# Kernel optimization log

Hardware: AMD Instinct MI355X
Metric: run time of the kernel (lower is better)

Reference implementation:

```python
import jax, jax.numpy as jnp
import numpy as np

N_NODES = 50000
N_EDGES = 262144
EMBED = 512
FF = 1024
N_GRAPHS = 64
EPS = 1e-12  # F.normalize default eps


def setup_inputs() -> dict:
    key = jax.random.key(0)
    ks = jax.random.split(key, 12)
    d_in = 3 * EMBED
    s1 = 1.0 / np.sqrt(d_in)
    s2 = 1.0 / np.sqrt(FF)
    return {
        "x": jax.random.normal(ks[0], (N_NODES + N_EDGES, EMBED), jnp.float32),
        "pos": jax.random.normal(ks[1], (N_NODES, 3), jnp.float32),
        "W1e": jax.random.uniform(ks[2], (d_in, FF), jnp.float32, -s1, s1),
        "b1e": jax.random.uniform(ks[3], (FF,), jnp.float32, -s1, s1),
        "W2e": jax.random.uniform(ks[4], (FF, 1), jnp.float32, -s2, s2),
        "b2e": jax.random.uniform(ks[5], (1,), jnp.float32, -s2, s2),
        "W1f": jax.random.uniform(ks[6], (d_in, FF), jnp.float32, -s1, s1),
        "b1f": jax.random.uniform(ks[7], (FF,), jnp.float32, -s1, s1),
        "W2f": jax.random.uniform(ks[8], (FF, 1), jnp.float32, -s2, s2),
        "b2f": jax.random.uniform(ks[9], (1,), jnp.float32, -s2, s2),
        "batch": jnp.sort(jax.random.randint(ks[10], (N_NODES,), 0, N_GRAPHS, jnp.int32)),
        "edge_index": jax.random.randint(ks[11], (2, N_EDGES), 0, N_NODES, jnp.int32),
    }


def _mlp(h, W1, b1, W2, b2):
    return jax.nn.gelu(h @ W1 + b1) @ W2 + b2


def reference(x, pos, W1e, b1e, W2e, b2e, W1f, b1f, W2f, b2f, batch, edge_index):
    n_nodes = pos.shape[0]
    n_edges = edge_index.shape[1]
    src, dst = edge_index[0], edge_index[1]
    # edge-token rows of x live right after the node rows
    edge_tok = jax.lax.dynamic_slice_in_dim(x, n_nodes, n_edges, axis=0)
    inputs = jnp.concatenate([x[src], x[dst], edge_tok], axis=-1)  # [E, 3*D]
    vec = pos[src] - pos[dst]  # [E, 3]
    norm = jnp.linalg.norm(vec, axis=-1, keepdims=True)
    vec_hat = vec / jnp.maximum(norm, EPS)
    energy_pairs = _mlp(inputs, W1e, b1e, W2e, b2e)            # [E, 1]
    force_pairs = _mlp(inputs, W1f, b1f, W2f, b2f) * vec_hat   # [E, 3]
    energy = jax.ops.segment_sum(energy_pairs, batch[src], num_segments=N_GRAPHS)
    forces = jax.ops.segment_sum(force_pairs, src, num_segments=n_nodes)
    return energy, forces
```

## Files before the change

### kernel.cpp

```cpp
#include <hip/hip_runtime.h>
#include <cstdint>
#include <cstddef>

#define E_CNT   262144
#define NNODES  50000
#define EMB     512
#define KD      1536
#define ND      2048
#define NG      64
#define XROWS   (NNODES + E_CNT)

typedef unsigned short u16;
typedef short  s8v __attribute__((ext_vector_type(8)));
typedef float  f4v __attribute__((ext_vector_type(4)));

#define WS_XB   0u
#define WS_WT   319635456u
#define WS_B1   325926912u
#define WS_W2   325935104u
#define WS_P    325943296u
#define WS_END  342720512u

__device__ __forceinline__ u16 f2bf(float f) {
    union { float f; uint32_t u; } v; v.f = f;
    uint32_t u = v.u;
    return (u16)((u + 0x7FFFu + ((u >> 16) & 1u)) >> 16);
}

__global__ void cvt_x(const float* __restrict__ x, uint32_t* __restrict__ xb) {
    size_t i = ((size_t)blockIdx.x * 256 + threadIdx.x) * 8;
    float4 a = *(const float4*)(x + i);
    float4 b = *(const float4*)(x + i + 4);
    uint4 r;
    r.x = (uint32_t)f2bf(a.x) | ((uint32_t)f2bf(a.y) << 16);
    r.y = (uint32_t)f2bf(a.z) | ((uint32_t)f2bf(a.w) << 16);
    r.z = (uint32_t)f2bf(b.x) | ((uint32_t)f2bf(b.y) << 16);
    r.w = (uint32_t)f2bf(b.z) | ((uint32_t)f2bf(b.w) << 16);
    *(uint4*)((char*)xb + i * 2) = r;
}

__global__ void prep_w(const float* __restrict__ W1e, const float* __restrict__ W1f,
                       u16* __restrict__ wt) {
    __shared__ float tile[32][33];
    int n0 = blockIdx.x * 32, k0 = blockIdx.y * 32;
    int tx = threadIdx.x & 31, ty = threadIdx.x >> 5;
#pragma unroll
    for (int i = 0; i < 4; ++i) {
        int k = k0 + ty + i * 8, n = n0 + tx;
        float v = (n < 1024) ? W1e[k * 1024 + n] : W1f[k * 1024 + (n - 1024)];
        tile[ty + i * 8][tx] = v;
    }
    __syncthreads();
#pragma unroll
    for (int i = 0; i < 4; ++i) {
        int nl = ty + i * 8, kl = tx;
        wt[(size_t)(n0 + nl) * KD + k0 + kl] = f2bf(tile[kl][nl]);
    }
}

__global__ void prep_small(const float* __restrict__ b1e, const float* __restrict__ b1f,
                           const float* __restrict__ W2e, const float* __restrict__ W2f,
                           float* __restrict__ b1c, float* __restrict__ w2c) {
    int n = blockIdx.x * 256 + threadIdx.x;
    if (n < 1024) { b1c[n] = b1e[n]; w2c[n] = W2e[n]; }
    else          { b1c[n] = b1f[n - 1024]; w2c[n] = W2f[n - 1024]; }
}

__global__ __launch_bounds__(256)
void gemm_mlp(const u16* __restrict__ xb, const u16* __restrict__ wt,
              const float* __restrict__ b1c, const float* __restrict__ w2c,
              const int* __restrict__ ei, float* __restrict__ P) {
    __shared__ u16 Al[2][128 * 64];
    __shared__ u16 Bl[2][128 * 64];
    __shared__ float part[128];

    const unsigned o = blockIdx.x + (blockIdx.y << 4);
    const int mb = (int)((o & 7u) + ((o >> 7) << 3));
    const int nb = (int)((o >> 3) & 15u);
    const int m0 = mb << 7;
    const int n0 = nb << 7;
    const int t  = threadIdx.x;
    const int l  = t & 63;
    const int w  = t >> 6;

    const int rbase = t >> 3;
    const int unit  = t & 7;
    const int sunit = (unit ^ (rbase & 7)) << 3;

    int srcs[4], dsts[4];
#pragma unroll
    for (int i = 0; i < 4; ++i) {
        int e = m0 + rbase + i * 32;
        srcs[i] = ei[e];
        dsts[i] = ei[E_CNT + e];
    }

    if (t < 128) part[t] = 0.0f;

    const int wm = (w & 1) << 6;
    const int wn = (w >> 1) << 6;

    float b1v[4], w2v[4];
#pragma unroll
    for (int nf = 0; nf < 4; ++nf) {
        int n = n0 + wn + nf * 16 + (l & 15);
        b1v[nf] = b1c[n];
        w2v[nf] = w2c[n];
    }

    f4v acc[4][4];
#pragma unroll
    for (int mf = 0; mf < 4; ++mf)
#pragma unroll
        for (int nf = 0; nf < 4; ++nf)
            acc[mf][nf] = (f4v){0.f, 0.f, 0.f, 0.f};

    auto stage = [&](u16* Ad, u16* Bd, int kt) {
        const int k0   = kt << 6;
        const int seg  = k0 >> 9;
        const int koff = k0 & 511;
#pragma unroll
        for (int i = 0; i < 4; ++i) {
            int row;
            if (seg == 0)      row = srcs[i];
            else if (seg == 1) row = dsts[i];
            else               row = NNODES + m0 + rbase + i * 32;
            const u16* g = xb + (size_t)row * EMB + koff + sunit;
            __builtin_amdgcn_global_load_lds(
                (const __attribute__((address_space(1))) void*)g,
                (__attribute__((address_space(3))) void*)(Ad + (i * 32 + w * 8) * 64),
                16, 0, 0);
        }
#pragma unroll
        for (int i = 0; i < 4; ++i) {
            int n = n0 + rbase + i * 32;
            const u16* g = wt + (size_t)n * KD + k0 + sunit;
            __builtin_amdgcn_global_load_lds(
                (const __attribute__((address_space(1))) void*)g,
                (__attribute__((address_space(3))) void*)(Bd + (i * 32 + w * 8) * 64),
                16, 0, 0);
        }
    };

    const int po0 = (((l >> 4) ^ (l & 7)) << 3);
    const int po1 = (((4 | (l >> 4)) ^ (l & 7)) << 3);

    const int l15 = l & 15;

    stage(Al[0], Bl[0], 0);
    __syncthreads();

    int cur = 0;
    for (int kt = 0; kt < 24; ++kt) {
        if (kt < 23) stage(Al[cur ^ 1], Bl[cur ^ 1], kt + 1);

        const u16* Ab = Al[cur];
        const u16* Bb = Bl[cur];
#pragma unroll
        for (int ks = 0; ks < 2; ++ks) {
            const int po = ks ? po1 : po0;
            s8v a[4], b[4];
#pragma unroll
            for (int mf = 0; mf < 4; ++mf)
                a[mf] = *(const s8v*)(Ab + (wm + mf * 16 + l15) * 64 + po);
#pragma unroll
            for (int nf = 0; nf < 4; ++nf)
                b[nf] = *(const s8v*)(Bb + (wn + nf * 16 + l15) * 64 + po);
            __builtin_amdgcn_s_setprio(1);
#pragma unroll
            for (int mf = 0; mf < 4; ++mf)
#pragma unroll
                for (int nf = 0; nf < 4; ++nf)
                    acc[mf][nf] = __builtin_amdgcn_mfma_f32_16x16x32_bf16(
                        a[mf], b[nf], acc[mf][nf], 0, 0, 0);
            __builtin_amdgcn_s_setprio(0);
        }
        __syncthreads();
        cur ^= 1;
    }

#pragma unroll
    for (int mf = 0; mf < 4; ++mf) {
#pragma unroll
        for (int r = 0; r < 4; ++r) {
            float s = 0.f;
#pragma unroll
            for (int nf = 0; nf < 4; ++nf) {
                float h  = acc[mf][nf][r] + b1v[nf];
                float x2 = h * h;
                float pp = fmaf(x2, 0.044715f, 1.0f);
                float u2 = 1.5957691216f * h * pp;
                float ex = __expf(-u2);
                float sg = __builtin_amdgcn_rcpf(1.0f + ex);
                s = fmaf(h * sg, w2v[nf], s);
            }
            s += __shfl_xor(s, 1);
            s += __shfl_xor(s, 2);
            s += __shfl_xor(s, 4);
            s += __shfl_xor(s, 8);
            if ((l & 15) == 0) {
                int m = wm + mf * 16 + ((l >> 4) << 2) + r;
                atomicAdd(&part[m], s);
            }
        }
    }
    __syncthreads();
    if (t < 128) P[(size_t)nb * E_CNT + m0 + t] = part[t];
}

__global__ void finalize(const float* __restrict__ P, const int* __restrict__ ei,
                         const float* __restrict__ pos, const int* __restrict__ batch,
                         const float* __restrict__ b2e, const float* __restrict__ b2f,
                         float* __restrict__ out) {
    __shared__ float ebin[NG];
    int t = threadIdx.x;
    if (t < NG) ebin[t] = 0.f;
    __syncthreads();
    int e = blockIdx.x * 256 + t;

    float se = b2e[0], sf = b2f[0];
#pragma unroll
    for (int nb = 0; nb < 8; ++nb)  se += P[(size_t)nb * E_CNT + e];
#pragma unroll
    for (int nb = 8; nb < 16; ++nb) sf += P[(size_t)nb * E_CNT + e];

    int s = ei[e], d = ei[E_CNT + e];
    float vx = pos[3 * s]     - pos[3 * d];
    float vy = pos[3 * s + 1] - pos[3 * d + 1];
    float vz = pos[3 * s + 2] - pos[3 * d + 2];
    float nrm = sqrtf(vx * vx + vy * vy + vz * vz);
    float inv = sf / fmaxf(nrm, 1e-12f);
    atomicAdd(&out[NG + 3 * s],     vx * inv);
    atomicAdd(&out[NG + 3 * s + 1], vy * inv);
    atomicAdd(&out[NG + 3 * s + 2], vz * inv);
    atomicAdd(&ebin[batch[s]], se);

    __syncthreads();
    if (t < NG) {
        float v = ebin[t];
        if (v != 0.f) atomicAdd(&out[t], v);
    }
}

extern "C" void kernel_launch(void* const* d_in, const int* in_sizes, int n_in,
                              void* d_out, int out_size, void* d_ws, size_t ws_size,
                              hipStream_t stream) {
    const float* x    = (const float*)d_in[0];
    const float* pos  = (const float*)d_in[1];
    const float* W1e  = (const float*)d_in[2];
    const float* b1e  = (const float*)d_in[3];
    const float* W2e  = (const float*)d_in[4];
    const float* b2e  = (const float*)d_in[5];
    const float* W1f  = (const float*)d_in[6];
    const float* b1f  = (const float*)d_in[7];
    const float* W2f  = (const float*)d_in[8];
    const float* b2f  = (const float*)d_in[9];
    const int*  batch = (const int*)d_in[10];
    const int*  ei    = (const int*)d_in[11];
    float* out        = (float*)d_out;

    if (ws_size < (size_t)WS_END) return;

    char* ws = (char*)d_ws;
    uint32_t* xb32 = (uint32_t*)(ws + WS_XB);
    u16*      xb   = (u16*)(ws + WS_XB);
    u16*      wt   = (u16*)(ws + WS_WT);
    float*    b1c  = (float*)(ws + WS_B1);
    float*    w2c  = (float*)(ws + WS_W2);
    float*    P    = (float*)(ws + WS_P);

    hipMemsetAsync(d_out, 0, (size_t)out_size * sizeof(float), stream);

    cvt_x<<<78036, 256, 0, stream>>>(x, xb32);
    prep_w<<<dim3(64, 48), 256, 0, stream>>>(W1e, W1f, wt);
    prep_small<<<8, 256, 0, stream>>>(b1e, b1f, W2e, W2f, b1c, w2c);
    gemm_mlp<<<dim3(16, 2048), 256, 0, stream>>>(xb, wt, b1c, w2c, ei, P);
    finalize<<<1024, 256, 0, stream>>>(P, ei, pos, batch, b2e, b2f, out);
}
```

Baseline: 3.228 ms.

## Triple-buffer LDS tiles with partial vmcnt waits in the fused GEMM-MLP

Replaces the double-buffered K loop with a three-stage LDS ring, so global-to-LDS loads run two tiles ahead. Each iteration now waits only for the oldest stage (vmcnt(8)) before a single barrier, instead of draining all loads and barrier-syncing at the end of every step. All LDS fragments for both k-substeps are loaded before the MFMA burst. The cost is more LDS per block (three A and three B buffers), and launch_bounds(256,1) signals one block per CU, which can lower occupancy and remove the latency hiding that came from co-resident blocks.

```diff
diff --git a/kernel.cpp b/kernel.cpp
--- a/kernel.cpp
+++ b/kernel.cpp
@@ -66,12 +66,12 @@
     else          { b1c[n] = b1f[n - 1024]; w2c[n] = W2f[n - 1024]; }
 }
 
-__global__ __launch_bounds__(256)
+__global__ __launch_bounds__(256, 1)
 void gemm_mlp(const u16* __restrict__ xb, const u16* __restrict__ wt,
               const float* __restrict__ b1c, const float* __restrict__ w2c,
               const int* __restrict__ ei, float* __restrict__ P) {
-    __shared__ u16 Al[2][128 * 64];
-    __shared__ u16 Bl[2][128 * 64];
+    __shared__ u16 Al[3][128 * 64];
+    __shared__ u16 Bl[3][128 * 64];
     __shared__ float part[128];
 
     const unsigned o = blockIdx.x + (blockIdx.y << 4);
@@ -144,40 +144,60 @@
 
     const int po0 = (((l >> 4) ^ (l & 7)) << 3);
     const int po1 = (((4 | (l >> 4)) ^ (l & 7)) << 3);
-
     const int l15 = l & 15;
 
-    stage(Al[0], Bl[0], 0);
-    __syncthreads();
-
-    int cur = 0;
-    for (int kt = 0; kt < 24; ++kt) {
-        if (kt < 23) stage(Al[cur ^ 1], Bl[cur ^ 1], kt + 1);
-
-        const u16* Ab = Al[cur];
-        const u16* Bb = Bl[cur];
-#pragma unroll
-        for (int ks = 0; ks < 2; ++ks) {
-            const int po = ks ? po1 : po0;
-            s8v a[4], b[4];
-#pragma unroll
-            for (int mf = 0; mf < 4; ++mf)
-                a[mf] = *(const s8v*)(Ab + (wm + mf * 16 + l15) * 64 + po);
-#pragma unroll
-            for (int nf = 0; nf < 4; ++nf)
-                b[nf] = *(const s8v*)(Bb + (wn + nf * 16 + l15) * 64 + po);
-            __builtin_amdgcn_s_setprio(1);
+    auto compute = [&](const u16* Ab, const u16* Bb) {
+        s8v a[2][4], b[2][4];
+#pragma unroll
+        for (int mf = 0; mf < 4; ++mf) {
+            a[0][mf] = *(const s8v*)(Ab + (wm + mf * 16 + l15) * 64 + po0);
+            a[1][mf] = *(const s8v*)(Ab + (wm + mf * 16 + l15) * 64 + po1);
+        }
+#pragma unroll
+        for (int nf = 0; nf < 4; ++nf) {
+            b[0][nf] = *(const s8v*)(Bb + (wn + nf * 16 + l15) * 64 + po0);
+            b[1][nf] = *(const s8v*)(Bb + (wn + nf * 16 + l15) * 64 + po1);
+        }
+        __builtin_amdgcn_s_setprio(1);
+#pragma unroll
+        for (int ks = 0; ks < 2; ++ks)
 #pragma unroll
             for (int mf = 0; mf < 4; ++mf)
 #pragma unroll
                 for (int nf = 0; nf < 4; ++nf)
                     acc[mf][nf] = __builtin_amdgcn_mfma_f32_16x16x32_bf16(
-                        a[mf], b[nf], acc[mf][nf], 0, 0, 0);
-            __builtin_amdgcn_s_setprio(0);
-        }
-        __syncthreads();
-        cur ^= 1;
-    }
+                        a[ks][mf], b[ks][nf], acc[mf][nf], 0, 0, 0);
+        __builtin_amdgcn_s_setprio(0);
+    };
+
+    u16 *Ac = Al[0], *An = Al[1], *As = Al[2];
+    u16 *Bc = Bl[0], *Bn = Bl[1], *Bs = Bl[2];
+
+    stage(Ac, Bc, 0);
+    stage(An, Bn, 1);
+    __syncthreads();
+
+    stage(As, Bs, 2);
+    compute(Ac, Bc);
+    { u16* tA = Ac; Ac = An; An = As; As = tA;
+      u16* tB = Bc; Bc = Bn; Bn = Bs; Bs = tB; }
+
+    for (int kt = 1; kt <= 21; ++kt) {
+        asm volatile("s_waitcnt vmcnt(8)" ::: "memory");
+        __builtin_amdgcn_s_barrier();
+        stage(As, Bs, kt + 2);
+        compute(Ac, Bc);
+        { u16* tA = Ac; Ac = An; An = As; As = tA;
+          u16* tB = Bc; Bc = Bn; Bn = Bs; Bs = tB; }
+    }
+    asm volatile("s_waitcnt vmcnt(8)" ::: "memory");
+    __builtin_amdgcn_s_barrier();
+    compute(Ac, Bc);
+    { u16* tA = Ac; Ac = An; An = As; As = tA;
+      u16* tB = Bc; Bc = Bn; Bn = Bs; Bs = tB; }
+    asm volatile("s_waitcnt vmcnt(0)" ::: "memory");
+    __builtin_amdgcn_s_barrier();
+    compute(Ac, Bc);
 
 #pragma unroll
     for (int mf = 0; mf < 4; ++mf) {
```

Result: slower. 3.586 ms (+11.1%).
